# Optimization experiments

Measured on AMD Instinct MI355X. Metric: run time of the kernel, lower is better.

Reference implementation:

```python
import jax, jax.numpy as jnp
import numpy as np

R_MAX = 6.0
P = 6.0
QQ = 14.399645 * 0.5  # metal units, * 0.5


def setup_inputs() -> dict:
    key = jax.random.key(0)
    k1, k2, k3, k4 = jax.random.split(key, 4)
    n_atoms = 100_000
    n_edges = 6_400_000
    num_types = 4
    # atomic numbers for H, C, O, Cu
    Z = jnp.asarray([1.0, 6.0, 8.0, 29.0], dtype=jnp.float32)
    # edge lengths in (0.1, 7.3) so some edges exceed r_max and get cut off
    r = jax.random.uniform(k1, (n_edges,), dtype=jnp.float32) * 7.2 + 0.1
    per_atom_energy = jax.random.normal(k2, (n_atoms, 1), dtype=jnp.float32)
    atom_types = jax.random.randint(k3, (n_atoms,), 0, num_types, dtype=jnp.int64)
    edge_index = jax.random.randint(k4, (2, n_edges), 0, n_atoms, dtype=jnp.int64)
    return {"Z": Z, "r": r, "per_atom_energy": per_atom_energy,
            "atom_types": atom_types, "edge_index": edge_index}


def _zbl_edge_energy(Z, r, atom_types, edge_index):
    pzbl = 0.23
    a0 = 0.4685
    c1, c2, c3, c4 = 0.02817, 0.28022, 0.50986, 0.18175
    d1, d2, d3, d4 = -0.20162, -0.4029, -0.94229, -3.1998
    edge_types = atom_types[edge_index]          # (2, E)
    Zpair = Z[edge_types]                        # (2, E)
    Zi, Zj = Zpair[0], Zpair[1]
    x = (jnp.power(Zi, pzbl) + jnp.power(Zj, pzbl)) * r / a0
    psi = (c1 * jnp.exp(d1 * x) + c2 * jnp.exp(d2 * x)
           + c3 * jnp.exp(d3 * x) + c4 * jnp.exp(d4 * x))
    eng = QQ * (Zi * Zj / r) * psi
    rr = r / R_MAX
    p = P
    cutoff = (1.0 - (p + 1.0) * (p + 2.0) / 2.0 * jnp.power(rr, p)
              + p * (p + 2.0) * jnp.power(rr, p + 1.0)
              - p * (p + 1.0) / 2.0 * jnp.power(rr, p + 2.0))
    cutoff = cutoff * (rr < 1.0).astype(cutoff.dtype)
    return cutoff * eng                          # (E,)


def reference(Z, r, per_atom_energy, atom_types, edge_index):
    edge_eng = _zbl_edge_energy(Z, r, atom_types, edge_index)
    n_atoms = per_atom_energy.shape[0]
    atomic_eng = jax.ops.segment_sum(edge_eng, edge_index[0],
                                     num_segments=n_atoms)[:, None]
    return atomic_eng + per_atom_energy
```

## Files before the change

### kernel.cpp

```cpp
#include <hip/hip_runtime.h>


namespace {
constexpr float PZBL     = 0.23f;
constexpr float A0_INV   = 1.0f / 0.4685f;
constexpr float C1 = 0.02817f, C2 = 0.28022f, C3 = 0.50986f, C4 = 0.18175f;
constexpr float D1 = -0.20162f, D2 = -0.4029f, D3 = -0.94229f, D4 = -3.1998f;
constexpr float QQ       = 14.399645f * 0.5f;
constexpr float RMAX     = 6.0f;
constexpr float RMAX_INV = 1.0f / 6.0f;
constexpr int   CHUNK    = 25600;
constexpr int   BLOCK    = 1024;
constexpr int   S_MAX    = 64;
constexpr int   TPW_MAX  = 6400;
}

__global__ void zbl_pack_types(const int* __restrict__ types,
                               unsigned* __restrict__ tpw,
                               int n_words, int n_atoms) {
    int w = blockIdx.x * blockDim.x + threadIdx.x;
    if (w >= n_words) return;
    unsigned v = 0;
    int base = w * 16;
    int m = min(16, n_atoms - base);
    for (int j = 0; j < m; ++j)
        v |= ((unsigned)types[base + j] & 3u) << (2 * j);
    tpw[w] = v;
}

__global__ __launch_bounds__(BLOCK) void zbl_chunk_kernel(
    const float*    __restrict__ Z,
    const float*    __restrict__ r,
    const int*      __restrict__ ei0,
    const int*      __restrict__ ei1,
    const unsigned* __restrict__ tpw,
    float*          __restrict__ partials,
    int n_chunks, int n_tp_words, int quads_per_slice,
    int n_quads, int n_edges) {
    __shared__ float    bins[CHUNK];
    __shared__ unsigned s_tp[TPW_MAX];
    __shared__ float    s_zz[16];
    __shared__ float    s_zx[16];

    const int tid = threadIdx.x;
    for (int i = tid; i < n_tp_words; i += BLOCK) s_tp[i] = tpw[i];
    if (tid < 16) {
        int ti = tid >> 2, tj = tid & 3;
        float zi = Z[ti], zj = Z[tj];
        s_zz[tid] = QQ * zi * zj;
        s_zx[tid] = (powf(zi, PZBL) + powf(zj, PZBL)) * A0_INV;
    }
    for (int i = tid; i < CHUNK; i += BLOCK) bins[i] = 0.0f;
    __syncthreads();

    const int c = blockIdx.x % n_chunks;
    const int s = blockIdx.x / n_chunks;
    const int base = c * CHUNK;

    auto edge = [&](float rk, int ia, int ib, unsigned d) {
        if (rk >= RMAX) return;
        unsigned ti = (s_tp[ia >> 4] >> ((ia & 15) * 2)) & 3u;
        unsigned tj = (s_tp[ib >> 4] >> ((ib & 15) * 2)) & 3u;
        int tp = (int)((ti << 2) | tj);
        float x = s_zx[tp] * rk;
        float psi = C1 * __expf(D1 * x) + C2 * __expf(D2 * x)
                  + C3 * __expf(D3 * x) + C4 * __expf(D4 * x);
        float eng = s_zz[tp] * psi * __builtin_amdgcn_rcpf(rk);
        float rr = rk * RMAX_INV;
        float rr2 = rr * rr;
        float rr3 = rr2 * rr;
        float rr6 = rr3 * rr3;
        float cutoff = 1.0f + rr6 * (-28.0f + rr * (48.0f - 21.0f * rr));
        atomicAdd(&bins[d], cutoff * eng);
    };

    const int q0 = s * quads_per_slice;
    const int q1 = min(n_quads, q0 + quads_per_slice);
    const float4* r4 = (const float4*)r;
    const int4*   a4 = (const int4*)ei0;
    const int4*   b4 = (const int4*)ei1;

    for (int q = q0 + tid; q < q1; q += BLOCK) {
        int4 av = a4[q];
        unsigned d0 = (unsigned)(av.x - base);
        unsigned d1 = (unsigned)(av.y - base);
        unsigned d2 = (unsigned)(av.z - base);
        unsigned d3 = (unsigned)(av.w - base);
        bool m0 = d0 < (unsigned)CHUNK, m1 = d1 < (unsigned)CHUNK;
        bool m2 = d2 < (unsigned)CHUNK, m3 = d3 < (unsigned)CHUNK;
        if (!(m0 | m1 | m2 | m3)) continue;
        float4 rv = r4[q];
        int4   bv = b4[q];
        if (m0) edge(rv.x, av.x, bv.x, d0);
        if (m1) edge(rv.y, av.y, bv.y, d1);
        if (m2) edge(rv.z, av.z, bv.z, d2);
        if (m3) edge(rv.w, av.w, bv.w, d3);
    }
    if (s == 0) {
        for (int e = 4 * n_quads + tid; e < n_edges; e += BLOCK) {
            int ia = ei0[e];
            unsigned d = (unsigned)(ia - base);
            if (d < (unsigned)CHUNK) edge(r[e], ia, ei1[e], d);
        }
    }
    __syncthreads();

    float* dst = partials + (size_t)blockIdx.x * CHUNK;
    for (int i = tid; i < CHUNK; i += BLOCK) dst[i] = bins[i];
}

__global__ void zbl_reduce_out(const float* __restrict__ pae,
                               const float* __restrict__ partials,
                               float* __restrict__ out,
                               int n_atoms, int n_chunks, int n_slices) {
    int a = blockIdx.x * blockDim.x + threadIdx.x;
    if (a >= n_atoms) return;
    int c = a / CHUNK;
    int i = a - c * CHUNK;
    const float* p = partials + (size_t)c * CHUNK + i;
    const size_t stride = (size_t)n_chunks * CHUNK;
    float s0 = 0.0f, s1 = 0.0f, s2 = 0.0f, s3 = 0.0f;
    int s = 0;
    for (; s + 4 <= n_slices; s += 4) {
        s0 += p[(size_t)(s + 0) * stride];
        s1 += p[(size_t)(s + 1) * stride];
        s2 += p[(size_t)(s + 2) * stride];
        s3 += p[(size_t)(s + 3) * stride];
    }
    for (; s < n_slices; ++s) s0 += p[(size_t)s * stride];
    out[a] = pae[a] + ((s0 + s1) + (s2 + s3));
}

__global__ void zbl_init_out(const float* __restrict__ pae,
                             float* __restrict__ out, int n) {
    int i = blockIdx.x * blockDim.x + threadIdx.x;
    if (i < n) out[i] = pae[i];
}

__global__ __launch_bounds__(256) void zbl_edge_fallback(
    const float* __restrict__ Z,
    const float* __restrict__ r,
    const int*   __restrict__ ei0,
    const int*   __restrict__ ei1,
    const int*   __restrict__ types,
    float*       __restrict__ out,
    int n_edges) {
    __shared__ float s_z[4];
    __shared__ float s_zp[4];
    if (threadIdx.x < 4) {
        float z = Z[threadIdx.x];
        s_z[threadIdx.x]  = z;
        s_zp[threadIdx.x] = powf(z, PZBL);
    }
    __syncthreads();
    int e = blockIdx.x * blockDim.x + threadIdx.x;
    if (e >= n_edges) return;
    float rk = r[e];
    if (rk >= RMAX) return;
    int ia = ei0[e], ib = ei1[e];
    int ti = types[ia], tj = types[ib];
    float x = (s_zp[ti] + s_zp[tj]) * rk * A0_INV;
    float psi = C1 * __expf(D1 * x) + C2 * __expf(D2 * x)
              + C3 * __expf(D3 * x) + C4 * __expf(D4 * x);
    float eng = QQ * s_z[ti] * s_z[tj] * psi / rk;
    float rr = rk * RMAX_INV;
    float rr2 = rr * rr, rr3 = rr2 * rr, rr6 = rr3 * rr3;
    float cutoff = 1.0f + rr6 * (-28.0f + rr * (48.0f - 21.0f * rr));
    unsafeAtomicAdd(&out[ia], cutoff * eng);
}

extern "C" void kernel_launch(void* const* d_in, const int* in_sizes, int n_in,
                              void* d_out, int out_size, void* d_ws, size_t ws_size,
                              hipStream_t stream) {
    const float* Z     = (const float*)d_in[0];
    const float* r     = (const float*)d_in[1];
    const float* pae   = (const float*)d_in[2];
    const int*   types = (const int*)d_in[3];
    const int*   ei    = (const int*)d_in[4];

    const int n_edges = in_sizes[1];
    const int n_atoms = in_sizes[2];

    float* out = (float*)d_out;

    const int n_chunks   = (n_atoms + CHUNK - 1) / CHUNK;
    const int n_tp_words = (n_atoms + 15) / 16;
    const int n_quads    = (n_edges & 3) ? 0 : (n_edges >> 2);

    const size_t tp_bytes    = ((size_t)n_tp_words * 4 + 15) & ~(size_t)15;
    const size_t part_floats = (size_t)n_chunks * S_MAX * CHUNK;

    const bool lds_path =
        n_tp_words <= TPW_MAX &&
        tp_bytes + part_floats * sizeof(float) <= ws_size;

    if (lds_path) {
        unsigned* tpw = (unsigned*)d_ws;
        float* partials = (float*)((char*)d_ws + tp_bytes);

        zbl_pack_types<<<(n_tp_words + 255) / 256, 256, 0, stream>>>(
            types, tpw, n_tp_words, n_atoms);

        const int quads_per_slice = (n_quads + S_MAX - 1) / S_MAX;
        zbl_chunk_kernel<<<n_chunks * S_MAX, BLOCK, 0, stream>>>(
            Z, r, ei, ei + n_edges, tpw, partials,
            n_chunks, n_tp_words, quads_per_slice, n_quads, n_edges);

        zbl_reduce_out<<<(n_atoms + 255) / 256, 256, 0, stream>>>(
            pae, partials, out, n_atoms, n_chunks, S_MAX);
    } else {
        zbl_init_out<<<(n_atoms + 255) / 256, 256, 0, stream>>>(pae, out, n_atoms);
        zbl_edge_fallback<<<(n_edges + 255) / 256, 256, 0, stream>>>(
            Z, r, ei, ei + n_edges, types, out, n_edges);
    }
}
```

Measured before the change: 166.9 us.

## Split edge energy computation and LDS binning into separate phases

Adds a two-phase path: first a grid-stride kernel computes each edge's energy once and writes an (atom index, energy) record, then a binning kernel with larger LDS chunks (3 chunks × up to 86 slices) scans the records and accumulates into shared-memory bins. Before, every chunk block re-read r/ei0/ei1 and re-computed nothing redundantly but re-read the index stream per chunk; now energy math is done once and binning reads compact 8-byte records. It adds a 51 MB record write plus re-reads per chunk, and needs more workspace; falls back to the old one-phase path otherwise.

Result: slower. 200.0 us (+19.8%).

```diff
diff --git a/kernel.cpp b/kernel.cpp
--- a/kernel.cpp
+++ b/kernel.cpp
@@ -9,10 +9,14 @@
 constexpr float QQ       = 14.399645f * 0.5f;
 constexpr float RMAX     = 6.0f;
 constexpr float RMAX_INV = 1.0f / 6.0f;
-constexpr int   CHUNK    = 25600;
+constexpr int   TPW_MAX  = 6400;
+constexpr int   P1_BLOCK = 256;
+constexpr int   P1_GRID  = 2048;
+constexpr int   CHUNK2   = 33344;
 constexpr int   BLOCK    = 1024;
-constexpr int   S_MAX    = 64;
-constexpr int   TPW_MAX  = 6400;
+constexpr int   S2_MAX   = 86;
+constexpr int   CHUNK1   = 25600;
+constexpr int   S1_MAX   = 64;
 }
 
 __global__ void zbl_pack_types(const int* __restrict__ types,
@@ -28,6 +32,137 @@
     tpw[w] = v;
 }
 
+__device__ __forceinline__ float edge_eng_lds(float rk, int ia, int ib,
+                                              const unsigned* s_tp,
+                                              const float* s_zz,
+                                              const float* s_zx) {
+    unsigned ti = (s_tp[ia >> 4] >> ((ia & 15) * 2)) & 3u;
+    unsigned tj = (s_tp[ib >> 4] >> ((ib & 15) * 2)) & 3u;
+    int tp = (int)((ti << 2) | tj);
+    float x = s_zx[tp] * rk;
+    float psi = C1 * __expf(D1 * x) + C2 * __expf(D2 * x)
+              + C3 * __expf(D3 * x) + C4 * __expf(D4 * x);
+    float eng = s_zz[tp] * psi * __builtin_amdgcn_rcpf(rk);
+    float rr = rk * RMAX_INV;
+    float rr2 = rr * rr;
+    float rr3 = rr2 * rr;
+    float rr6 = rr3 * rr3;
+    float cutoff = 1.0f + rr6 * (-28.0f + rr * (48.0f - 21.0f * rr));
+    return (rk < RMAX) ? cutoff * eng : 0.0f;
+}
+
+__global__ __launch_bounds__(P1_BLOCK) void zbl_energy_kernel(
+    const float*    __restrict__ Z,
+    const float*    __restrict__ r,
+    const int*      __restrict__ ei0,
+    const int*      __restrict__ ei1,
+    const unsigned* __restrict__ tpw,
+    int4*           __restrict__ rec4,
+    int2*           __restrict__ rec2,
+    int n_tp_words, int n_quads, int n_edges) {
+    __shared__ unsigned s_tp[TPW_MAX];
+    __shared__ float    s_zz[16];
+    __shared__ float    s_zx[16];
+
+    const int tid = threadIdx.x;
+    for (int i = tid; i < n_tp_words; i += P1_BLOCK) s_tp[i] = tpw[i];
+    if (tid < 16) {
+        int ti = tid >> 2, tj = tid & 3;
+        float zi = Z[ti], zj = Z[tj];
+        s_zz[tid] = QQ * zi * zj;
+        s_zx[tid] = (powf(zi, PZBL) + powf(zj, PZBL)) * A0_INV;
+    }
+    __syncthreads();
+
+    const float4* r4 = (const float4*)r;
+    const int4*   a4 = (const int4*)ei0;
+    const int4*   b4 = (const int4*)ei1;
+    const int stride = gridDim.x * P1_BLOCK;
+
+    for (int q = blockIdx.x * P1_BLOCK + tid; q < n_quads; q += stride) {
+        float4 rv = r4[q];
+        int4   av = a4[q];
+        int4   bv = b4[q];
+        float e0 = edge_eng_lds(rv.x, av.x, bv.x, s_tp, s_zz, s_zx);
+        float e1 = edge_eng_lds(rv.y, av.y, bv.y, s_tp, s_zz, s_zx);
+        float e2 = edge_eng_lds(rv.z, av.z, bv.z, s_tp, s_zz, s_zx);
+        float e3 = edge_eng_lds(rv.w, av.w, bv.w, s_tp, s_zz, s_zx);
+        rec4[2 * q]     = make_int4(av.x, __float_as_int(e0),
+                                    av.y, __float_as_int(e1));
+        rec4[2 * q + 1] = make_int4(av.z, __float_as_int(e2),
+                                    av.w, __float_as_int(e3));
+    }
+    if (blockIdx.x == 0) {
+        for (int e = 4 * n_quads + tid; e < n_edges; e += P1_BLOCK) {
+            int ia = ei0[e];
+            rec2[e] = make_int2(
+                ia, __float_as_int(edge_eng_lds(r[e], ia, ei1[e],
+                                                s_tp, s_zz, s_zx)));
+        }
+    }
+}
+
+__global__ __launch_bounds__(BLOCK) void zbl_bin_kernel(
+    const int4* __restrict__ rec4,
+    const int2* __restrict__ rec2,
+    float*      __restrict__ partials,
+    int n_chunks, int i4_per_slice, int n_i4, int n_records) {
+    __shared__ float bins[CHUNK2];
+    for (int i = threadIdx.x; i < CHUNK2; i += BLOCK) bins[i] = 0.0f;
+    __syncthreads();
+
+    const int c = blockIdx.x % n_chunks;
+    const int s = blockIdx.x / n_chunks;
+    const int base = c * CHUNK2;
+
+    const int q0 = s * i4_per_slice;
+    const int q1 = min(n_i4, q0 + i4_per_slice);
+    for (int q = q0 + threadIdx.x; q < q1; q += BLOCK) {
+        int4 p = rec4[q];
+        unsigned d0 = (unsigned)(p.x - base);
+        unsigned d1 = (unsigned)(p.z - base);
+        if (d0 < (unsigned)CHUNK2 && p.y != 0)
+            atomicAdd(&bins[d0], __int_as_float(p.y));
+        if (d1 < (unsigned)CHUNK2 && p.w != 0)
+            atomicAdd(&bins[d1], __int_as_float(p.w));
+    }
+    if (s == 0) {
+        for (int e = 2 * n_i4 + threadIdx.x; e < n_records; e += BLOCK) {
+            int2 p = rec2[e];
+            unsigned d = (unsigned)(p.x - base);
+            if (d < (unsigned)CHUNK2 && p.y != 0)
+                atomicAdd(&bins[d], __int_as_float(p.y));
+        }
+    }
+    __syncthreads();
+
+    float* dst = partials + (size_t)blockIdx.x * CHUNK2;
+    for (int i = threadIdx.x; i < CHUNK2; i += BLOCK) dst[i] = bins[i];
+}
+
+__global__ void zbl_reduce_out(const float* __restrict__ pae,
+                               const float* __restrict__ partials,
+                               float* __restrict__ out,
+                               int n_atoms, int n_chunks, int n_slices,
+                               int chunk) {
+    int a = blockIdx.x * blockDim.x + threadIdx.x;
+    if (a >= n_atoms) return;
+    int c = a / chunk;
+    int i = a - c * chunk;
+    const float* p = partials + (size_t)c * chunk + i;
+    const size_t stride = (size_t)n_chunks * chunk;
+    float s0 = 0.0f, s1 = 0.0f, s2 = 0.0f, s3 = 0.0f;
+    int s = 0;
+    for (; s + 4 <= n_slices; s += 4) {
+        s0 += p[(size_t)(s + 0) * stride];
+        s1 += p[(size_t)(s + 1) * stride];
+        s2 += p[(size_t)(s + 2) * stride];
+        s3 += p[(size_t)(s + 3) * stride];
+    }
+    for (; s < n_slices; ++s) s0 += p[(size_t)s * stride];
+    out[a] = pae[a] + ((s0 + s1) + (s2 + s3));
+}
+
 __global__ __launch_bounds__(BLOCK) void zbl_chunk_kernel(
     const float*    __restrict__ Z,
     const float*    __restrict__ r,
@@ -37,11 +172,10 @@
     float*          __restrict__ partials,
     int n_chunks, int n_tp_words, int quads_per_slice,
     int n_quads, int n_edges) {
-    __shared__ float    bins[CHUNK];
+    __shared__ float    bins[CHUNK1];
     __shared__ unsigned s_tp[TPW_MAX];
     __shared__ float    s_zz[16];
     __shared__ float    s_zx[16];
-
     const int tid = threadIdx.x;
     for (int i = tid; i < n_tp_words; i += BLOCK) s_tp[i] = tpw[i];
     if (tid < 16) {
@@ -50,85 +184,46 @@
         s_zz[tid] = QQ * zi * zj;
         s_zx[tid] = (powf(zi, PZBL) + powf(zj, PZBL)) * A0_INV;
     }
-    for (int i = tid; i < CHUNK; i += BLOCK) bins[i] = 0.0f;
-    __syncthreads();
-
+    for (int i = tid; i < CHUNK1; i += BLOCK) bins[i] = 0.0f;
+    __syncthreads();
     const int c = blockIdx.x % n_chunks;
     const int s = blockIdx.x / n_chunks;
-    const int base = c * CHUNK;
-
-    auto edge = [&](float rk, int ia, int ib, unsigned d) {
-        if (rk >= RMAX) return;
-        unsigned ti = (s_tp[ia >> 4] >> ((ia & 15) * 2)) & 3u;
-        unsigned tj = (s_tp[ib >> 4] >> ((ib & 15) * 2)) & 3u;
-        int tp = (int)((ti << 2) | tj);
-        float x = s_zx[tp] * rk;
-        float psi = C1 * __expf(D1 * x) + C2 * __expf(D2 * x)
-                  + C3 * __expf(D3 * x) + C4 * __expf(D4 * x);
-        float eng = s_zz[tp] * psi * __builtin_amdgcn_rcpf(rk);
-        float rr = rk * RMAX_INV;
-        float rr2 = rr * rr;
-        float rr3 = rr2 * rr;
-        float rr6 = rr3 * rr3;
-        float cutoff = 1.0f + rr6 * (-28.0f + rr * (48.0f - 21.0f * rr));
-        atomicAdd(&bins[d], cutoff * eng);
-    };
-
+    const int base = c * CHUNK1;
     const int q0 = s * quads_per_slice;
     const int q1 = min(n_quads, q0 + quads_per_slice);
-    const float4* r4 = (const float4*)r;
-    const int4*   a4 = (const int4*)ei0;
-    const int4*   b4 = (const int4*)ei1;
-
     for (int q = q0 + tid; q < q1; q += BLOCK) {
-        int4 av = a4[q];
+        int4 av = ((const int4*)ei0)[q];
         unsigned d0 = (unsigned)(av.x - base);
         unsigned d1 = (unsigned)(av.y - base);
         unsigned d2 = (unsigned)(av.z - base);
         unsigned d3 = (unsigned)(av.w - base);
-        bool m0 = d0 < (unsigned)CHUNK, m1 = d1 < (unsigned)CHUNK;
-        bool m2 = d2 < (unsigned)CHUNK, m3 = d3 < (unsigned)CHUNK;
+        bool m0 = d0 < (unsigned)CHUNK1, m1 = d1 < (unsigned)CHUNK1;
+        bool m2 = d2 < (unsigned)CHUNK1, m3 = d3 < (unsigned)CHUNK1;
         if (!(m0 | m1 | m2 | m3)) continue;
-        float4 rv = r4[q];
-        int4   bv = b4[q];
-        if (m0) edge(rv.x, av.x, bv.x, d0);
-        if (m1) edge(rv.y, av.y, bv.y, d1);
-        if (m2) edge(rv.z, av.z, bv.z, d2);
-        if (m3) edge(rv.w, av.w, bv.w, d3);
+        float4 rv = ((const float4*)r)[q];
+        int4   bv = ((const int4*)ei1)[q];
+        if (m0) { float e = edge_eng_lds(rv.x, av.x, bv.x, s_tp, s_zz, s_zx);
+                  if (e != 0.0f) atomicAdd(&bins[d0], e); }
+        if (m1) { float e = edge_eng_lds(rv.y, av.y, bv.y, s_tp, s_zz, s_zx);
+                  if (e != 0.0f) atomicAdd(&bins[d1], e); }
+        if (m2) { float e = edge_eng_lds(rv.z, av.z, bv.z, s_tp, s_zz, s_zx);
+                  if (e != 0.0f) atomicAdd(&bins[d2], e); }
+        if (m3) { float e = edge_eng_lds(rv.w, av.w, bv.w, s_tp, s_zz, s_zx);
+                  if (e != 0.0f) atomicAdd(&bins[d3], e); }
     }
     if (s == 0) {
         for (int e = 4 * n_quads + tid; e < n_edges; e += BLOCK) {
             int ia = ei0[e];
             unsigned d = (unsigned)(ia - base);
-            if (d < (unsigned)CHUNK) edge(r[e], ia, ei1[e], d);
+            if (d < (unsigned)CHUNK1) {
+                float e2 = edge_eng_lds(r[e], ia, ei1[e], s_tp, s_zz, s_zx);
+                if (e2 != 0.0f) atomicAdd(&bins[d], e2);
+            }
         }
     }
     __syncthreads();
-
-    float* dst = partials + (size_t)blockIdx.x * CHUNK;
-    for (int i = tid; i < CHUNK; i += BLOCK) dst[i] = bins[i];
-}
-
-__global__ void zbl_reduce_out(const float* __restrict__ pae,
-                               const float* __restrict__ partials,
-                               float* __restrict__ out,
-                               int n_atoms, int n_chunks, int n_slices) {
-    int a = blockIdx.x * blockDim.x + threadIdx.x;
-    if (a >= n_atoms) return;
-    int c = a / CHUNK;
-    int i = a - c * CHUNK;
-    const float* p = partials + (size_t)c * CHUNK + i;
-    const size_t stride = (size_t)n_chunks * CHUNK;
-    float s0 = 0.0f, s1 = 0.0f, s2 = 0.0f, s3 = 0.0f;
-    int s = 0;
-    for (; s + 4 <= n_slices; s += 4) {
-        s0 += p[(size_t)(s + 0) * stride];
-        s1 += p[(size_t)(s + 1) * stride];
-        s2 += p[(size_t)(s + 2) * stride];
-        s3 += p[(size_t)(s + 3) * stride];
-    }
-    for (; s < n_slices; ++s) s0 += p[(size_t)s * stride];
-    out[a] = pae[a] + ((s0 + s1) + (s2 + s3));
+    float* dst = partials + (size_t)blockIdx.x * CHUNK1;
+    for (int i = tid; i < CHUNK1; i += BLOCK) dst[i] = bins[i];
 }
 
 __global__ void zbl_init_out(const float* __restrict__ pae,
@@ -183,31 +278,65 @@
 
     float* out = (float*)d_out;
 
-    const int n_chunks   = (n_atoms + CHUNK - 1) / CHUNK;
     const int n_tp_words = (n_atoms + 15) / 16;
     const int n_quads    = (n_edges & 3) ? 0 : (n_edges >> 2);
 
-    const size_t tp_bytes    = ((size_t)n_tp_words * 4 + 15) & ~(size_t)15;
-    const size_t part_floats = (size_t)n_chunks * S_MAX * CHUNK;
-
-    const bool lds_path =
+    const size_t tp_bytes  = ((size_t)n_tp_words * 4 + 15) & ~(size_t)15;
+    const size_t rec_bytes = ((size_t)n_edges * 8 + 15) & ~(size_t)15;
+
+    const int nc2 = (n_atoms + CHUNK2 - 1) / CHUNK2;
+    int S2 = S2_MAX;
+    while (S2 > 4 &&
+           tp_bytes + rec_bytes +
+           (size_t)nc2 * S2 * CHUNK2 * sizeof(float) > ws_size) {
+        --S2;
+    }
+    const bool two_phase =
         n_tp_words <= TPW_MAX &&
-        tp_bytes + part_floats * sizeof(float) <= ws_size;
-
-    if (lds_path) {
+        tp_bytes + rec_bytes + (size_t)nc2 * S2 * CHUNK2 * sizeof(float)
+            <= ws_size;
+
+    const int nc1 = (n_atoms + CHUNK1 - 1) / CHUNK1;
+    const bool one_phase =
+        n_tp_words <= TPW_MAX &&
+        tp_bytes + (size_t)nc1 * S1_MAX * CHUNK1 * sizeof(float) <= ws_size;
+
+    if (two_phase) {
+        unsigned* tpw = (unsigned*)d_ws;
+        int2* rec2 = (int2*)((char*)d_ws + tp_bytes);
+        int4* rec4 = (int4*)rec2;
+        float* partials = (float*)((char*)d_ws + tp_bytes + rec_bytes);
+
+        zbl_pack_types<<<(n_tp_words + 255) / 256, 256, 0, stream>>>(
+            types, tpw, n_tp_words, n_atoms);
+
+        int p1_grid = n_quads ? min(P1_GRID, (n_quads + P1_BLOCK - 1) / P1_BLOCK)
+                              : 1;
+        zbl_energy_kernel<<<p1_grid, P1_BLOCK, 0, stream>>>(
+            Z, r, ei, ei + n_edges, tpw, rec4, rec2,
+            n_tp_words, n_quads, n_edges);
+
+        const int n_i4 = n_edges >> 1;
+        const int i4_per_slice = (n_i4 + S2 - 1) / S2;
+        zbl_bin_kernel<<<nc2 * S2, BLOCK, 0, stream>>>(
+            rec4, rec2, partials, nc2, i4_per_slice, n_i4, n_edges);
+
+        zbl_reduce_out<<<(n_atoms + 255) / 256, 256, 0, stream>>>(
+            pae, partials, out, n_atoms, nc2, S2, CHUNK2);
+    } else if (one_phase) {
         unsigned* tpw = (unsigned*)d_ws;
         float* partials = (float*)((char*)d_ws + tp_bytes);
 
         zbl_pack_types<<<(n_tp_words + 255) / 256, 256, 0, stream>>>(
             types, tpw, n_tp_words, n_atoms);
 
-        const int quads_per_slice = (n_quads + S_MAX - 1) / S_MAX;
-        zbl_chunk_kernel<<<n_chunks * S_MAX, BLOCK, 0, stream>>>(
+        const int quads_per_slice = (n_quads + S1_MAX - 1) / S1_MAX;
+        zbl_chunk_kernel<<<nc1 * S1_MAX, BLOCK, 0, stream>>>(
             Z, r, ei, ei + n_edges, tpw, partials,
-            n_chunks, n_tp_words, quads_per_slice, n_quads, n_edges);
+            nc1, n_tp_words, quads_per_slice, n_quads, n_edges);
 
         zbl_reduce_out<<<(n_atoms + 255) / 256, 256, 0, stream>>>(
-            pae, partials, out, n_atoms, n_chunks, S_MAX);
+            pae, partials, out, n_atoms, nc1, S1_MAX, CHUNK1);
     } else {
         zbl_init_out<<<(n_atoms + 255) / 256, 256, 0, stream>>>(pae, out, n_atoms);
         zbl_edge_fallback<<<(n_edges + 255) / 256, 256, 0, stream>>>(
```
